# Performance work log

Hardware: AMD Instinct MI355X
Metric: run time of the kernel (lower is better)

The kernel has to match this reference:

```python
import jax, jax.numpy as jnp
import numpy as np

N = 256
FEAT = 1024           # box_head.fc7.out_features
HID_REL = 256         # RelationProposalNetwork hidden_dim
GCN_HID = 256         # gcn_hidden
HEADS = 4
NUM_PARTS = 20
OUT = NUM_PARTS + 1
TOPK = 3
IN_GCN = FEAT + 4


def setup_inputs() -> dict:
    key = jax.random.key(0)
    ks = jax.random.split(key, 16)
    features = jax.random.normal(ks[0], (N, FEAT), jnp.float32)
    # valid pixel-space boxes (x1, y1, x2, y2) inside an 800x800 image
    xy = jax.random.uniform(ks[1], (N, 2), jnp.float32, 0.0, 700.0)
    wh = jax.random.uniform(ks[2], (N, 2), jnp.float32, 8.0, 100.0)
    boxes = jnp.concatenate([xy, xy + wh], axis=1)
    s = 0.02
    W_fc1 = jax.random.normal(ks[3], (2 * FEAT + 4, HID_REL), jnp.float32) * s
    b_fc1 = jnp.zeros((HID_REL,), jnp.float32)
    W_fc2 = jax.random.normal(ks[4], (HID_REL, 1), jnp.float32) * s
    b_fc2 = jnp.zeros((1,), jnp.float32)
    W1 = jax.random.normal(ks[5], (IN_GCN, HEADS * GCN_HID), jnp.float32) * s
    a_src1 = jax.random.normal(ks[6], (HEADS, GCN_HID), jnp.float32) * s
    a_dst1 = jax.random.normal(ks[7], (HEADS, GCN_HID), jnp.float32) * s
    b1 = jnp.zeros((HEADS * GCN_HID,), jnp.float32)
    W2 = jax.random.normal(ks[8], (HEADS * GCN_HID, OUT), jnp.float32) * s
    a_src2 = jax.random.normal(ks[9], (1, OUT), jnp.float32) * s
    a_dst2 = jax.random.normal(ks[10], (1, OUT), jnp.float32) * s
    b2 = jnp.zeros((OUT,), jnp.float32)
    return {
        "features": features, "boxes": boxes,
        "W_fc1": W_fc1, "b_fc1": b_fc1, "W_fc2": W_fc2, "b_fc2": b_fc2,
        "W1": W1, "a_src1": a_src1, "a_dst1": a_dst1, "b1": b1,
        "W2": W2, "a_src2": a_src2, "a_dst2": a_dst2, "b2": b2,
        "img_h": 800, "img_w": 800,
    }


def _gat_layer(x, W, a_src, a_dst, bias, s, t, n, heads, ch):
    # PyG GATConv: message flows edge_index[0] (s) -> edge_index[1] (t),
    # softmax over incoming edges of each target node t.
    h = (x @ W).reshape(n, heads, ch)                       # [n, H, C]
    e = jax.nn.leaky_relu(
        jnp.einsum("ehc,hc->eh", h[s], a_src)
        + jnp.einsum("ehc,hc->eh", h[t], a_dst), 0.2)        # [E, H]
    m = jnp.full((n, heads), -1e30, e.dtype).at[t].max(e)    # segment max
    p = jnp.exp(e - m[t])
    denom = jax.ops.segment_sum(p, t, num_segments=n)
    alpha = p / denom[t]                                     # [E, H]
    out = jax.ops.segment_sum(alpha[:, :, None] * h[s], t, num_segments=n)
    return out.reshape(n, heads * ch) + bias


def _forward(features, boxes, W_fc1, b_fc1, W_fc2, b_fc2,
             W1, a_src1, a_dst1, b1, W2, a_src2, a_dst2, b2, img_h, img_w):
    n = features.shape[0]
    # --- RelationProposalNetwork: dense O(N^2) pairwise MLP ---
    f1 = jnp.broadcast_to(features[:, None, :], (n, n, FEAT))
    f2 = jnp.broadcast_to(features[None, :, :], (n, n, FEAT))
    geom = jnp.abs(boxes[:, None, :] - boxes[None, :, :])    # [n, n, 4]
    pair = jnp.concatenate([f1, f2, geom], axis=-1)          # [n, n, 2052]
    hid = jax.nn.relu(pair @ W_fc1 + b_fc1)                  # [n, n, 256]
    rel = (hid @ W_fc2 + b_fc2)[..., 0]                      # [n, n]
    # --- top-k graph construction (drop first = self, as in source) ---
    idx = jax.lax.top_k(rel, TOPK + 1)[1][:, 1:]             # [n, topk]
    s_e = jnp.repeat(jnp.arange(n), TOPK)                    # edge_index[0]
    t_e = idx.reshape(-1)                                    # edge_index[1]
    loops = jnp.arange(n)                                    # GATConv add_self_loops
    s_e = jnp.concatenate([s_e, loops])
    t_e = jnp.concatenate([t_e, loops])
    # --- normalized box geometry node features ---
    scale = jnp.array([img_w, img_h, img_w, img_h], jnp.float32)
    nb = boxes / scale
    geomn = jnp.stack([nb[:, 0], nb[:, 1], nb[:, 2] - nb[:, 0], nb[:, 3] - nb[:, 1]], axis=1)
    gcn_in = jnp.concatenate([features, geomn], axis=1)      # [n, 1028]
    # --- AttentionalGCN: GAT(heads=4) -> ReLU -> GAT(heads=1) ---
    h1 = jax.nn.relu(_gat_layer(gcn_in, W1, a_src1, a_dst1, b1, s_e, t_e, n, HEADS, GCN_HID))
    logits = _gat_layer(h1, W2, a_src2, a_dst2, b2, s_e, t_e, n, 1, OUT)
    return logits


def reference(features, boxes, W_fc1, b_fc1, W_fc2, b_fc2,
              W1, a_src1, a_dst1, b1, W2, a_src2, a_dst2, b2, img_h, img_w):
    logits = _forward(features, boxes, W_fc1, b_fc1, W_fc2, b_fc2,
                      W1, a_src1, a_dst1, b1, W2, a_src2, a_dst2, b2, img_h, img_w)
    labels = jnp.argmax(logits, axis=1)
    return logits, labels
```

## Files before the change

kernel.cpp:

```cpp
#include <hip/hip_runtime.h>
#include <math.h>

#define NN 256
#define FEAT 1024
#define HIDR 256
#define HEADS 4
#define GCNH 256
#define M1 1024
#define OUTC 21
#define MAXDEG (NN + 1)
#define KC 16
#define KCH (FEAT / KC)
#define RB 16
#define FCOLS 1536

__device__ __forceinline__ void st_wt4(float* p, float4 v) {
    union { float4 f; unsigned long long u[2]; } cv; cv.f = v;
    __hip_atomic_store((unsigned long long*)p, cv.u[0],
                       __ATOMIC_RELAXED, __HIP_MEMORY_SCOPE_AGENT);
    __hip_atomic_store((unsigned long long*)p + 1, cv.u[1],
                       __ATOMIC_RELAXED, __HIP_MEMORY_SCOPE_AGENT);
}
__device__ __forceinline__ void st_wtf(float* p, float v) {
    __hip_atomic_store((unsigned*)p, __float_as_uint(v),
                       __ATOMIC_RELAXED, __HIP_MEMORY_SCOPE_AGENT);
}
__device__ __forceinline__ void st_wti(int* p, int v) {
    __hip_atomic_store(p, v, __ATOMIC_RELAXED, __HIP_MEMORY_SCOPE_AGENT);
}

__global__ __launch_bounds__(256) void k_big(
        const float* __restrict__ feat, const float* __restrict__ Wfc1,
        const float* __restrict__ W1, float* __restrict__ P,
        unsigned* bar) {
    if (blockIdx.x == 0 && blockIdx.y == 0 && blockIdx.z == 0 &&
        threadIdx.x == 0)
        __hip_atomic_store(bar, 0u, __ATOMIC_RELAXED, __HIP_MEMORY_SCOPE_AGENT);
    __shared__ float fS[RB][KCH];
    int rg = blockIdx.x, cgy = blockIdx.y, kc = blockIdx.z;
    int tid = threadIdx.x;
    int r0 = rg * RB, k0 = kc * KCH;
    for (int x = tid; x < RB * KCH; x += 256) {
        int r = x >> 6, kk = x & (KCH - 1);
        fS[r][kk] = feat[(size_t)(r0 + r) * FEAT + k0 + kk];
    }
    __syncthreads();
    int gc = cgy * 512 + tid * 2;
    const float* pW;
    int ld;
    if (gc < 256)      { pW = Wfc1 + (size_t)k0 * HIDR + gc;                  ld = HIDR; }
    else if (gc < 512) { pW = Wfc1 + (size_t)(FEAT + k0) * HIDR + (gc - 256); ld = HIDR; }
    else               { pW = W1   + (size_t)k0 * M1 + (gc - 512);            ld = M1;   }
    float2 acc[RB];
#pragma unroll
    for (int r = 0; r < RB; r++) { acc[r].x = 0.f; acc[r].y = 0.f; }
    float2 w0 = *(const float2*)(pW);
    float2 w1 = *(const float2*)(pW + ld);
    float2 w2 = *(const float2*)(pW + 2 * ld);
    float2 w3 = *(const float2*)(pW + 3 * ld);
    for (int kk = 0; kk < KCH; kk += 4) {
        pW += 4 * ld;
        float2 n0 = *(const float2*)(pW);
        float2 n1 = *(const float2*)(pW + ld);
        float2 n2 = *(const float2*)(pW + 2 * ld);
        float2 n3 = *(const float2*)(pW + 3 * ld);
#pragma unroll
        for (int r = 0; r < RB; r++) {
            float4 f = *(const float4*)&fS[r][kk];
            acc[r].x = fmaf(f.x, w0.x, acc[r].x); acc[r].y = fmaf(f.x, w0.y, acc[r].y);
            acc[r].x = fmaf(f.y, w1.x, acc[r].x); acc[r].y = fmaf(f.y, w1.y, acc[r].y);
            acc[r].x = fmaf(f.z, w2.x, acc[r].x); acc[r].y = fmaf(f.z, w2.y, acc[r].y);
            acc[r].x = fmaf(f.w, w3.x, acc[r].x); acc[r].y = fmaf(f.w, w3.y, acc[r].y);
        }
        w0 = n0; w1 = n1; w2 = n2; w3 = n3;
    }
    float* Pp = P + ((size_t)kc * NN + r0) * FCOLS + gc;
#pragma unroll
    for (int r = 0; r < RB; r++)
        *(float2*)(Pp + (size_t)r * FCOLS) = acc[r];
}

__device__ __forceinline__ void gsync(unsigned* bar, unsigned expected) {
    __syncthreads();
    if (threadIdx.x == 0) {
        __hip_atomic_fetch_add(bar, 1u, __ATOMIC_RELAXED,
                               __HIP_MEMORY_SCOPE_AGENT);
        while (__hip_atomic_load(bar, __ATOMIC_RELAXED,
                                 __HIP_MEMORY_SCOPE_AGENT) < expected)
            __builtin_amdgcn_s_sleep(16);
        __builtin_amdgcn_fence(__ATOMIC_ACQUIRE, "agent");
    }
    __syncthreads();
}

__global__ __launch_bounds__(512, 4) void k_fused(
        const float* __restrict__ P, const float* __restrict__ bfc1,
        const float* __restrict__ boxes, const int* __restrict__ imh,
        const int* __restrict__ imw, const float* __restrict__ W1,
        const float* __restrict__ as1, const float* __restrict__ ad1,
        const float* __restrict__ Wfc1, const float* __restrict__ Wfc2,
        const float* __restrict__ b1, const float* __restrict__ W2,
        const float* __restrict__ as2, const float* __restrict__ ad2,
        const float* __restrict__ b2,
        float* __restrict__ BT4, float* __restrict__ hpre,
        float* __restrict__ es1, float* __restrict__ ed1,
        int* __restrict__ idxTop, float* __restrict__ h2,
        float* __restrict__ es2, float* __restrict__ ed2,
        unsigned* bar, float* __restrict__ out) {
    __shared__ float gS[4];
    __shared__ float As[HIDR], w2s[HIDR];
    __shared__ float wg0[HIDR], wg1[HIDR], wg2[HIDR], wg3[HIDR];
    __shared__ float sval[512];
    __shared__ unsigned long long swk[8];
    __shared__ int win;
    __shared__ int pfx[NN];
    __shared__ int lst[MAXDEG];
    __shared__ int dgS;
    __shared__ float sc[MAXDEG * 4];
    __shared__ float mh[4], dh[4];
    __shared__ float sh[M1];
    __shared__ float part[24 * OUTC];
    __shared__ float h2row[OUTC];
    __shared__ float scD[MAXDEG];
    __shared__ float md[2];
    __shared__ float lv[OUTC];

    int row = blockIdx.x, tid = threadIdx.x;

    int c4 = tid * 4;
    bool actA = (tid < 384);
    float4 s4;
    if (actA) {
        const float* p = P + (size_t)row * FCOLS + c4;
        const size_t str = (size_t)NN * FCOLS;
        float4 a0 = *(const float4*)(p);
        float4 a1 = *(const float4*)(p + str);
        float4 a2 = *(const float4*)(p + 2 * str);
        float4 a3 = *(const float4*)(p + 3 * str);
#pragma unroll
        for (int q = 4; q < KC; q += 4) {
            float4 t0 = *(const float4*)(p + (size_t)q * str);
            float4 t1 = *(const float4*)(p + (size_t)(q + 1) * str);
            float4 t2 = *(const float4*)(p + (size_t)(q + 2) * str);
            float4 t3 = *(const float4*)(p + (size_t)(q + 3) * str);
            a0.x += t0.x; a0.y += t0.y; a0.z += t0.z; a0.w += t0.w;
            a1.x += t1.x; a1.y += t1.y; a1.z += t1.z; a1.w += t1.w;
            a2.x += t2.x; a2.y += t2.y; a2.z += t2.z; a2.w += t2.w;
            a3.x += t3.x; a3.y += t3.y; a3.z += t3.z; a3.w += t3.w;
        }
        s4.x = (a0.x + a1.x) + (a2.x + a3.x);
        s4.y = (a0.y + a1.y) + (a2.y + a3.y);
        s4.z = (a0.z + a1.z) + (a2.z + a3.z);
        s4.w = (a0.w + a1.w) + (a2.w + a3.w);
    }
    if (tid == 0) {
        float w = (float)imw[0], h = (float)imh[0];
        float x1 = boxes[row * 4 + 0] / w, y1 = boxes[row * 4 + 1] / h;
        float x2 = boxes[row * 4 + 2] / w, y2 = boxes[row * 4 + 3] / h;
        gS[0] = x1; gS[1] = y1; gS[2] = x2 - x1; gS[3] = y2 - y1;
    }
    __syncthreads();
    if (actA) {
        if (c4 < 256) {
            float4 b = *(const float4*)(bfc1 + c4);
            s4.x += b.x; s4.y += b.y; s4.z += b.z; s4.w += b.w;
            *(float4*)(&As[c4]) = s4;
        } else if (c4 < 512) {
            int kk = c4 - 256;
            st_wt4(BT4 + (size_t)(kk >> 2) * (NN * 4) + row * 4, s4);
        } else {
            int ch = c4 - 512;
            float g0 = gS[0], g1 = gS[1], g2 = gS[2], g3 = gS[3];
            float4 wv;
            wv = *(const float4*)(W1 + (size_t)(FEAT + 0) * M1 + ch);
            s4.x = fmaf(g0, wv.x, s4.x); s4.y = fmaf(g0, wv.y, s4.y);
            s4.z = fmaf(g0, wv.z, s4.z); s4.w = fmaf(g0, wv.w, s4.w);
            wv = *(const float4*)(W1 + (size_t)(FEAT + 1) * M1 + ch);
            s4.x = fmaf(g1, wv.x, s4.x); s4.y = fmaf(g1, wv.y, s4.y);
            s4.z = fmaf(g1, wv.z, s4.z); s4.w = fmaf(g1, wv.w, s4.w);
            wv = *(const float4*)(W1 + (size_t)(FEAT + 2) * M1 + ch);
            s4.x = fmaf(g2, wv.x, s4.x); s4.y = fmaf(g2, wv.y, s4.y);
            s4.z = fmaf(g2, wv.z, s4.z); s4.w = fmaf(g2, wv.w, s4.w);
            wv = *(const float4*)(W1 + (size_t)(FEAT + 3) * M1 + ch);
            s4.x = fmaf(g3, wv.x, s4.x); s4.y = fmaf(g3, wv.y, s4.y);
            s4.z = fmaf(g3, wv.z, s4.z); s4.w = fmaf(g3, wv.w, s4.w);
            st_wt4(hpre + (size_t)row * M1 + ch, s4);
            float4 a = *(const float4*)(as1 + ch);
            float4 b = *(const float4*)(ad1 + ch);
            float ps = s4.x * a.x + s4.y * a.y + s4.z * a.z + s4.w * a.w;
            float pd = s4.x * b.x + s4.y * b.y + s4.z * b.z + s4.w * b.w;
#pragma unroll
            for (int o = 32; o > 0; o >>= 1) {
                ps += __shfl_down(ps, o);
                pd += __shfl_down(pd, o);
            }
            if ((tid & 63) == 0) {
                int head = (tid - 128) >> 6;
                st_wtf(es1 + row * 4 + head, ps);
                st_wtf(ed1 + row * 4 + head, pd);
            }
        }
    }

    gsync(bar, NN);

    if (tid < 256) {
        w2s[tid] = Wfc2[tid];
        wg0[tid] = Wfc1[(size_t)(2 * FEAT + 0) * HIDR + tid];
    } else {
        int q = tid - 256;
        wg1[q] = Wfc1[(size_t)(2 * FEAT + 1) * HIDR + q];
        wg2[q] = Wfc1[(size_t)(2 * FEAT + 2) * HIDR + q];
        wg3[q] = Wfc1[(size_t)(2 * FEAT + 3) * HIDR + q];
    }
    int j = tid & 255, half = tid >> 8;
    float bi0 = boxes[row * 4 + 0], bi1 = boxes[row * 4 + 1];
    float bi2 = boxes[row * 4 + 2], bi3 = boxes[row * 4 + 3];
    float g0 = fabsf(bi0 - boxes[j * 4 + 0]);
    float g1 = fabsf(bi1 - boxes[j * 4 + 1]);
    float g2 = fabsf(bi2 - boxes[j * 4 + 2]);
    float g3 = fabsf(bi3 - boxes[j * 4 + 3]);
    __syncthreads();
    {
        int k0 = half * 128;
        const float* pB = BT4 + (size_t)(k0 >> 2) * (NN * 4) + j * 4;
        float acc = 0.f;
#pragma unroll 4
        for (int kk = k0; kk < k0 + 128; kk += 4) {
            float4 a4 = *(const float4*)&As[kk];
            float4 w4 = *(const float4*)&w2s[kk];
            float4 q0 = *(const float4*)&wg0[kk];
            float4 q1 = *(const float4*)&wg1[kk];
            float4 q2 = *(const float4*)&wg2[kk];
            float4 q3 = *(const float4*)&wg3[kk];
            float4 b4 = *(const float4*)pB;
            pB += NN * 4;
            float v;
            v = a4.x + b4.x; v = fmaf(g0, q0.x, v); v = fmaf(g1, q1.x, v);
            v = fmaf(g2, q2.x, v); v = fmaf(g3, q3.x, v);
            acc = fmaf(fmaxf(v, 0.f), w4.x, acc);
            v = a4.y + b4.y; v = fmaf(g0, q0.y, v); v = fmaf(g1, q1.y, v);
            v = fmaf(g2, q2.y, v); v = fmaf(g3, q3.y, v);
            acc = fmaf(fmaxf(v, 0.f), w4.y, acc);
            v = a4.z + b4.z; v = fmaf(g0, q0.z, v); v = fmaf(g1, q1.z, v);
            v = fmaf(g2, q2.z, v); v = fmaf(g3, q3.z, v);
            acc = fmaf(fmaxf(v, 0.f), w4.z, acc);
            v = a4.w + b4.w; v = fmaf(g0, q0.w, v); v = fmaf(g1, q1.w, v);
            v = fmaf(g2, q2.w, v); v = fmaf(g3, q3.w, v);
            acc = fmaf(fmaxf(v, 0.f), w4.w, acc);
        }
        sval[tid] = acc;
    }
    __syncthreads();
    if (tid < 256) sval[tid] = sval[tid] + sval[tid + 256];
    __syncthreads();
    for (int r = 0; r < 4; r++) {
        unsigned long long key = 0ULL;
        if (tid < 256) {
            unsigned u = __float_as_uint(sval[tid]);
            u = (u & 0x80000000u) ? ~u : (u | 0x80000000u);
            key = ((unsigned long long)u << 32) | (unsigned)(NN - 1 - tid);
        }
#pragma unroll
        for (int o = 32; o > 0; o >>= 1) {
            unsigned long long nk = __shfl_down(key, o);
            if (nk > key) key = nk;
        }
        if ((tid & 63) == 0) swk[tid >> 6] = key;
        __syncthreads();
        if (tid == 0) {
            unsigned long long m = swk[0];
#pragma unroll
            for (int q = 1; q < 8; q++) if (swk[q] > m) m = swk[q];
            int wj = NN - 1 - (int)(m & 0xFFFFFFFFu);
            win = wj;
            if (r > 0) st_wti(idxTop + row * 3 + (r - 1), wj);
        }
        __syncthreads();
        if (tid == win) sval[tid] = -1e38f;
        __syncthreads();
    }

    gsync(bar, 2 * NN);

    int f = 0;
    if (tid < 256) {
        f = (idxTop[tid * 3 + 0] == row) | (idxTop[tid * 3 + 1] == row)
          | (idxTop[tid * 3 + 2] == row);
        pfx[tid] = f;
    }
    __syncthreads();
    for (int o = 1; o < NN; o <<= 1) {
        int add = 0;
        if (tid < 256 && tid >= o) add = pfx[tid - o];
        __syncthreads();
        if (tid < 256) pfx[tid] += add;
        __syncthreads();
    }
    if (tid < 256 && f) lst[pfx[tid] - 1] = tid;
    if (tid == NN - 1) {
        int d = pfx[NN - 1];
        lst[d] = row;
        dgS = d + 1;
    }
    __syncthreads();
    int dg = dgS;
    for (int p = tid; p < dg * 4; p += 512) {
        int e = p >> 2, hq = p & 3;
        int s = lst[e];
        float v = es1[s * 4 + hq] + ed1[row * 4 + hq];
        sc[p] = v >= 0.f ? v : 0.2f * v;
    }
    __syncthreads();
    {
        int hq = tid & 3;
        float lm = -1e30f;
        for (int e = tid >> 2; e < dg; e += 128)
            lm = fmaxf(lm, sc[e * 4 + hq]);
        sval[tid] = lm;
        __syncthreads();
        for (int o = 256; o >= 4; o >>= 1) {
            if (tid < o) sval[tid] = fmaxf(sval[tid], sval[tid + o]);
            __syncthreads();
        }
        if (tid < 4) mh[tid] = sval[tid];
        __syncthreads();
        float m = mh[hq];
        float lsum = 0.f;
        for (int e = tid >> 2; e < dg; e += 128) {
            float pv = expf(sc[e * 4 + hq] - m);
            sc[e * 4 + hq] = pv;
            lsum += pv;
        }
        sval[tid] = lsum;
        __syncthreads();
        for (int o = 256; o >= 4; o >>= 1) {
            if (tid < o) sval[tid] += sval[tid + o];
            __syncthreads();
        }
        if (tid < 4) dh[tid] = sval[tid];
        __syncthreads();
        for (int p = tid; p < dg * 4; p += 512)
            sc[p] = sc[p] / dh[p & 3];
    }
    __syncthreads();
    {
        int col = tid & 255, hh = (tid >> 8) * 2;
        float acc0 = 0.f, acc1 = 0.f;
        int e = 0;
        for (; e + 8 <= dg; e += 8) {
            float v0[8], v1[8];
#pragma unroll
            for (int u = 0; u < 8; u++) {
                const float* hs = hpre + (size_t)lst[e + u] * M1;
                v0[u] = hs[hh * GCNH + col];
                v1[u] = hs[(hh + 1) * GCNH + col];
            }
#pragma unroll
            for (int u = 0; u < 8; u++) {
                acc0 = fmaf(sc[(e + u) * 4 + hh],     v0[u], acc0);
                acc1 = fmaf(sc[(e + u) * 4 + hh + 1], v1[u], acc1);
            }
        }
        for (; e < dg; e++) {
            const float* hs = hpre + (size_t)lst[e] * M1;
            acc0 = fmaf(sc[e * 4 + hh],     hs[hh * GCNH + col],       acc0);
            acc1 = fmaf(sc[e * 4 + hh + 1], hs[(hh + 1) * GCNH + col], acc1);
        }
        int c0 = hh * GCNH + col, c1 = (hh + 1) * GCNH + col;
        sh[c0] = fmaxf(acc0 + b1[c0], 0.f);
        sh[c1] = fmaxf(acc1 + b1[c1], 0.f);
    }
    __syncthreads();
    if (tid < 504) {
        int o = tid % OUTC, pq = tid / OUTC;
        float a2 = 0.f;
        for (int d = pq; d < M1; d += 24)
            a2 = fmaf(sh[d], W2[d * OUTC + o], a2);
        part[pq * OUTC + o] = a2;
    }
    __syncthreads();
    if (tid < OUTC) {
        float ssum = 0.f;
        for (int pq = 0; pq < 24; pq++) ssum += part[pq * OUTC + tid];
        st_wtf(h2 + row * OUTC + tid, ssum);
        h2row[tid] = ssum;
    }
    __syncthreads();
    if (tid == 0) {
        float ssum = 0.f, dd = 0.f;
        for (int k = 0; k < OUTC; k++) {
            ssum = fmaf(h2row[k], as2[k], ssum);
            dd = fmaf(h2row[k], ad2[k], dd);
        }
        st_wtf(es2 + row, ssum);
        st_wtf(ed2 + row, dd);
    }

    gsync(bar, 3 * NN);

    int dgT = dgS;
    float edt = ed2[row];
    for (int p = tid; p < dgT; p += 512) {
        int s = lst[p];
        float v = es2[s] + edt;
        scD[p] = v >= 0.f ? v : 0.2f * v;
    }
    __syncthreads();
    {
        float lm = -1e30f;
        for (int p = tid; p < dgT; p += 512) lm = fmaxf(lm, scD[p]);
        sval[tid] = lm;
        __syncthreads();
        for (int o = 256; o >= 1; o >>= 1) {
            if (tid < o) sval[tid] = fmaxf(sval[tid], sval[tid + o]);
            __syncthreads();
        }
        if (tid == 0) md[0] = sval[0];
        __syncthreads();
        float m = md[0];
        float lsum = 0.f;
        for (int p = tid; p < dgT; p += 512) {
            float pv = expf(scD[p] - m);
            scD[p] = pv;
            lsum += pv;
        }
        sval[tid] = lsum;
        __syncthreads();
        for (int o = 256; o >= 1; o >>= 1) {
            if (tid < o) sval[tid] += sval[tid + o];
            __syncthreads();
        }
        if (tid == 0) md[1] = sval[0];
        __syncthreads();
    }
    if (tid < 504) {
        int o = tid % OUTC, eg = tid / OUTC;
        float acc = 0.f;
        for (int e = eg; e < dgT; e += 24) {
            int s = lst[e];
            acc = fmaf(scD[e], h2[(size_t)s * OUTC + o], acc);
        }
        part[eg * OUTC + o] = acc;
    }
    __syncthreads();
    if (tid < OUTC) {
        float ssum = 0.f;
        for (int eg = 0; eg < 24; eg++) ssum += part[eg * OUTC + tid];
        float v = ssum / md[1] + b2[tid];
        out[row * OUTC + tid] = v;
        lv[tid] = v;
    }
    __syncthreads();
    if (tid == 0) {
        int best = 0;
        float bv = lv[0];
        for (int o = 1; o < OUTC; o++)
            if (lv[o] > bv) { bv = lv[o]; best = o; }
        out[NN * OUTC + row] = (float)best;
    }
}

extern "C" void kernel_launch(void* const* d_in, const int* in_sizes, int n_in,
                              void* d_out, int out_size, void* d_ws,
                              size_t ws_size, hipStream_t stream) {
    const float* feat  = (const float*)d_in[0];
    const float* boxes = (const float*)d_in[1];
    const float* Wfc1  = (const float*)d_in[2];
    const float* bfc1  = (const float*)d_in[3];
    const float* Wfc2  = (const float*)d_in[4];
    const float* bfc2  = (const float*)d_in[5];   (void)bfc2;
    const float* W1    = (const float*)d_in[6];
    const float* as1   = (const float*)d_in[7];
    const float* ad1   = (const float*)d_in[8];
    const float* b1    = (const float*)d_in[9];
    const float* W2    = (const float*)d_in[10];
    const float* as2   = (const float*)d_in[11];
    const float* ad2   = (const float*)d_in[12];
    const float* b2    = (const float*)d_in[13];
    const int*   imh   = (const int*)d_in[14];
    const int*   imw   = (const int*)d_in[15];

    float* ws = (float*)d_ws;
    float* P     = ws;  ws += KC * NN * FCOLS;
    float* BT4   = ws;  ws += NN * HIDR;
    float* hpre  = ws;  ws += NN * M1;
    float* es1   = ws;  ws += NN * 4;
    float* ed1   = ws;  ws += NN * 4;
    float* h2    = ws;  ws += NN * OUTC;
    float* es2   = ws;  ws += NN;
    float* ed2   = ws;  ws += NN;
    int* idxTop  = (int*)ws;  ws += NN * 3;
    unsigned* bar = (unsigned*)ws;

    float* out = (float*)d_out;

    k_big<<<dim3(NN / RB, 3, KC), 256, 0, stream>>>(feat, Wfc1, W1, P, bar);
    k_fused<<<NN, 512, 0, stream>>>(P, bfc1, boxes, imh, imw, W1, as1, ad1,
                                    Wfc1, Wfc2, b1, W2, as2, ad2, b2,
                                    BT4, hpre, es1, ed1, idxTop, h2, es2, ed2,
                                    bar, out);
}
```

Baseline: 157.6 us.

## Fuse split-K GEMM into persistent kernel and use wave-level reductions

The separate split-K GEMM kernel becomes the first phase of the persistent cooperative kernel, with an extra grid barrier; each block now reads features straight from global memory instead of staging them in LDS, and handles three column groups. The barrier is reset with a memset instead of inside the first kernel. The barrier spin sleep is shortened, and the shared-memory tree reductions and prefix scan are replaced by wave shuffles and ballot/popcount. This removes one launch and many __syncthreads, but adds a grid barrier and changes the GEMM tiling and memory access pattern.

New measurement: 186.2 us. +18.1%, slower.

```diff
diff --git a/kernel.cpp b/kernel.cpp
--- a/kernel.cpp
+++ b/kernel.cpp
@@ -4,7 +4,6 @@
 #define NN 256
 #define FEAT 1024
 #define HIDR 256
-#define HEADS 4
 #define GCNH 256
 #define M1 1024
 #define OUTC 21
@@ -29,57 +28,6 @@
     __hip_atomic_store(p, v, __ATOMIC_RELAXED, __HIP_MEMORY_SCOPE_AGENT);
 }
 
-__global__ __launch_bounds__(256) void k_big(
-        const float* __restrict__ feat, const float* __restrict__ Wfc1,
-        const float* __restrict__ W1, float* __restrict__ P,
-        unsigned* bar) {
-    if (blockIdx.x == 0 && blockIdx.y == 0 && blockIdx.z == 0 &&
-        threadIdx.x == 0)
-        __hip_atomic_store(bar, 0u, __ATOMIC_RELAXED, __HIP_MEMORY_SCOPE_AGENT);
-    __shared__ float fS[RB][KCH];
-    int rg = blockIdx.x, cgy = blockIdx.y, kc = blockIdx.z;
-    int tid = threadIdx.x;
-    int r0 = rg * RB, k0 = kc * KCH;
-    for (int x = tid; x < RB * KCH; x += 256) {
-        int r = x >> 6, kk = x & (KCH - 1);
-        fS[r][kk] = feat[(size_t)(r0 + r) * FEAT + k0 + kk];
-    }
-    __syncthreads();
-    int gc = cgy * 512 + tid * 2;
-    const float* pW;
-    int ld;
-    if (gc < 256)      { pW = Wfc1 + (size_t)k0 * HIDR + gc;                  ld = HIDR; }
-    else if (gc < 512) { pW = Wfc1 + (size_t)(FEAT + k0) * HIDR + (gc - 256); ld = HIDR; }
-    else               { pW = W1   + (size_t)k0 * M1 + (gc - 512);            ld = M1;   }
-    float2 acc[RB];
-#pragma unroll
-    for (int r = 0; r < RB; r++) { acc[r].x = 0.f; acc[r].y = 0.f; }
-    float2 w0 = *(const float2*)(pW);
-    float2 w1 = *(const float2*)(pW + ld);
-    float2 w2 = *(const float2*)(pW + 2 * ld);
-    float2 w3 = *(const float2*)(pW + 3 * ld);
-    for (int kk = 0; kk < KCH; kk += 4) {
-        pW += 4 * ld;
-        float2 n0 = *(const float2*)(pW);
-        float2 n1 = *(const float2*)(pW + ld);
-        float2 n2 = *(const float2*)(pW + 2 * ld);
-        float2 n3 = *(const float2*)(pW + 3 * ld);
-#pragma unroll
-        for (int r = 0; r < RB; r++) {
-            float4 f = *(const float4*)&fS[r][kk];
-            acc[r].x = fmaf(f.x, w0.x, acc[r].x); acc[r].y = fmaf(f.x, w0.y, acc[r].y);
-            acc[r].x = fmaf(f.y, w1.x, acc[r].x); acc[r].y = fmaf(f.y, w1.y, acc[r].y);
-            acc[r].x = fmaf(f.z, w2.x, acc[r].x); acc[r].y = fmaf(f.z, w2.y, acc[r].y);
-            acc[r].x = fmaf(f.w, w3.x, acc[r].x); acc[r].y = fmaf(f.w, w3.y, acc[r].y);
-        }
-        w0 = n0; w1 = n1; w2 = n2; w3 = n3;
-    }
-    float* Pp = P + ((size_t)kc * NN + r0) * FCOLS + gc;
-#pragma unroll
-    for (int r = 0; r < RB; r++)
-        *(float2*)(Pp + (size_t)r * FCOLS) = acc[r];
-}
-
 __device__ __forceinline__ void gsync(unsigned* bar, unsigned expected) {
     __syncthreads();
     if (threadIdx.x == 0) {
@@ -87,45 +35,91 @@
                                __HIP_MEMORY_SCOPE_AGENT);
         while (__hip_atomic_load(bar, __ATOMIC_RELAXED,
                                  __HIP_MEMORY_SCOPE_AGENT) < expected)
-            __builtin_amdgcn_s_sleep(16);
+            __builtin_amdgcn_s_sleep(2);
         __builtin_amdgcn_fence(__ATOMIC_ACQUIRE, "agent");
     }
     __syncthreads();
 }
 
-__global__ __launch_bounds__(512, 4) void k_fused(
-        const float* __restrict__ P, const float* __restrict__ bfc1,
-        const float* __restrict__ boxes, const int* __restrict__ imh,
-        const int* __restrict__ imw, const float* __restrict__ W1,
+__global__ __launch_bounds__(512, 4) void k_all(
+        const float* __restrict__ feat, const float* __restrict__ boxes,
+        const float* __restrict__ Wfc1, const float* __restrict__ bfc1,
+        const float* __restrict__ Wfc2, const float* __restrict__ W1,
         const float* __restrict__ as1, const float* __restrict__ ad1,
-        const float* __restrict__ Wfc1, const float* __restrict__ Wfc2,
         const float* __restrict__ b1, const float* __restrict__ W2,
         const float* __restrict__ as2, const float* __restrict__ ad2,
-        const float* __restrict__ b2,
-        float* __restrict__ BT4, float* __restrict__ hpre,
-        float* __restrict__ es1, float* __restrict__ ed1,
-        int* __restrict__ idxTop, float* __restrict__ h2,
-        float* __restrict__ es2, float* __restrict__ ed2,
-        unsigned* bar, float* __restrict__ out) {
+        const float* __restrict__ b2, const int* __restrict__ imh,
+        const int* __restrict__ imw,
+        float* __restrict__ P, float* __restrict__ BT4,
+        float* __restrict__ hpre, float* __restrict__ es1,
+        float* __restrict__ ed1, int* __restrict__ idxTop,
+        float* __restrict__ h2, float* __restrict__ es2,
+        float* __restrict__ ed2, unsigned* bar, float* __restrict__ out) {
     __shared__ float gS[4];
     __shared__ float As[HIDR], w2s[HIDR];
     __shared__ float wg0[HIDR], wg1[HIDR], wg2[HIDR], wg3[HIDR];
     __shared__ float sval[512];
     __shared__ unsigned long long swk[8];
     __shared__ int win;
-    __shared__ int pfx[NN];
+    __shared__ int pfxw[4];
     __shared__ int lst[MAXDEG];
     __shared__ int dgS;
     __shared__ float sc[MAXDEG * 4];
-    __shared__ float mh[4], dh[4];
     __shared__ float sh[M1];
     __shared__ float part[24 * OUTC];
     __shared__ float h2row[OUTC];
     __shared__ float scD[MAXDEG];
-    __shared__ float md[2];
     __shared__ float lv[OUTC];
 
-    int row = blockIdx.x, tid = threadIdx.x;
+    int b = blockIdx.x, tid = threadIdx.x;
+
+    {
+        int rg = b & 15, kc = b >> 4;
+        int r0 = rg * RB, k0 = kc * KCH;
+        const float* p0 = (tid < 256)
+            ? Wfc1 + (size_t)k0 * HIDR + tid
+            : Wfc1 + (size_t)(FEAT + k0) * HIDR + (tid - 256);
+        const float* p1 = W1 + (size_t)k0 * M1 + tid;
+        const float* p2 = p1 + 512;
+        float acc0[RB], acc1[RB], acc2[RB];
+#pragma unroll
+        for (int r = 0; r < RB; r++) { acc0[r] = 0.f; acc1[r] = 0.f; acc2[r] = 0.f; }
+        const float* fbp = feat + (size_t)r0 * FEAT + k0;
+        for (int kb = 0; kb < KCH; kb += 8) {
+            float w0[8], w1[8], w2[8];
+#pragma unroll
+            for (int k = 0; k < 8; k++) {
+                w0[k] = p0[(size_t)k * HIDR];
+                w1[k] = p1[(size_t)k * M1];
+                w2[k] = p2[(size_t)k * M1];
+            }
+            p0 += 8 * HIDR; p1 += 8 * M1; p2 += 8 * M1;
+#pragma unroll
+            for (int r = 0; r < RB; r++) {
+                const float* fr = fbp + (size_t)r * FEAT + kb;
+                float4 fa = *(const float4*)(fr);
+                float4 fc = *(const float4*)(fr + 4);
+                float fv[8] = {fa.x, fa.y, fa.z, fa.w, fc.x, fc.y, fc.z, fc.w};
+#pragma unroll
+                for (int k = 0; k < 8; k++) {
+                    acc0[r] = fmaf(fv[k], w0[k], acc0[r]);
+                    acc1[r] = fmaf(fv[k], w1[k], acc1[r]);
+                    acc2[r] = fmaf(fv[k], w2[k], acc2[r]);
+                }
+            }
+        }
+        float* Pp = P + ((size_t)kc * NN + r0) * FCOLS;
+#pragma unroll
+        for (int r = 0; r < RB; r++) {
+            st_wtf(Pp + (size_t)r * FCOLS + tid,        acc0[r]);
+            st_wtf(Pp + (size_t)r * FCOLS + 512 + tid,  acc1[r]);
+            st_wtf(Pp + (size_t)r * FCOLS + 1024 + tid, acc2[r]);
+        }
+    }
+
+    gsync(bar, NN);
+
+    int row = b;
 
     int c4 = tid * 4;
     bool actA = (tid < 384);
@@ -162,8 +156,8 @@
     __syncthreads();
     if (actA) {
         if (c4 < 256) {
-            float4 b = *(const float4*)(bfc1 + c4);
-            s4.x += b.x; s4.y += b.y; s4.z += b.z; s4.w += b.w;
+            float4 bv = *(const float4*)(bfc1 + c4);
+            s4.x += bv.x; s4.y += bv.y; s4.z += bv.z; s4.w += bv.w;
             *(float4*)(&As[c4]) = s4;
         } else if (c4 < 512) {
             int kk = c4 - 256;
@@ -186,9 +180,9 @@
             s4.z = fmaf(g3, wv.z, s4.z); s4.w = fmaf(g3, wv.w, s4.w);
             st_wt4(hpre + (size_t)row * M1 + ch, s4);
             float4 a = *(const float4*)(as1 + ch);
-            float4 b = *(const float4*)(ad1 + ch);
+            float4 bv = *(const float4*)(ad1 + ch);
             float ps = s4.x * a.x + s4.y * a.y + s4.z * a.z + s4.w * a.w;
-            float pd = s4.x * b.x + s4.y * b.y + s4.z * b.z + s4.w * b.w;
+            float pd = s4.x * bv.x + s4.y * bv.y + s4.z * bv.z + s4.w * bv.w;
 #pragma unroll
             for (int o = 32; o > 0; o >>= 1) {
                 ps += __shfl_down(ps, o);
@@ -202,7 +196,7 @@
         }
     }
 
-    gsync(bar, NN);
+    gsync(bar, 2 * NN);
 
     if (tid < 256) {
         w2s[tid] = Wfc2[tid];
@@ -281,67 +275,64 @@
         __syncthreads();
     }
 
-    gsync(bar, 2 * NN);
+    gsync(bar, 3 * NN);
 
     int f = 0;
-    if (tid < 256) {
+    if (tid < 256)
         f = (idxTop[tid * 3 + 0] == row) | (idxTop[tid * 3 + 1] == row)
           | (idxTop[tid * 3 + 2] == row);
-        pfx[tid] = f;
-    }
-    __syncthreads();
-    for (int o = 1; o < NN; o <<= 1) {
-        int add = 0;
-        if (tid < 256 && tid >= o) add = pfx[tid - o];
-        __syncthreads();
-        if (tid < 256) pfx[tid] += add;
-        __syncthreads();
-    }
-    if (tid < 256 && f) lst[pfx[tid] - 1] = tid;
-    if (tid == NN - 1) {
-        int d = pfx[NN - 1];
-        lst[d] = row;
-        dgS = d + 1;
+    unsigned long long bm = __ballot(f);
+    int lane = tid & 63, wv6 = tid >> 6;
+    int rank = __popcll(bm & ((1ULL << lane) - 1ULL));
+    if (tid < 256 && lane == 0) pfxw[wv6] = __popcll(bm);
+    __syncthreads();
+    {
+        int base = 0;
+#pragma unroll
+        for (int w = 0; w < 4; w++) base += (w < wv6) ? pfxw[w] : 0;
+        if (tid < 256 && f) lst[base + rank] = tid;
+    }
+    if (tid == 0) {
+        int tot = pfxw[0] + pfxw[1] + pfxw[2] + pfxw[3];
+        lst[tot] = row;
+        dgS = tot + 1;
     }
     __syncthreads();
     int dg = dgS;
     for (int p = tid; p < dg * 4; p += 512) {
-        int e = p >> 2, hq = p & 3;
+        int e = p >> 2, hq2 = p & 3;
         int s = lst[e];
-        float v = es1[s * 4 + hq] + ed1[row * 4 + hq];
+        float v = es1[s * 4 + hq2] + ed1[row * 4 + hq2];
         sc[p] = v >= 0.f ? v : 0.2f * v;
     }
     __syncthreads();
-    {
-        int hq = tid & 3;
+    int hq = tid & 3;
+    {
         float lm = -1e30f;
         for (int e = tid >> 2; e < dg; e += 128)
             lm = fmaxf(lm, sc[e * 4 + hq]);
-        sval[tid] = lm;
-        __syncthreads();
-        for (int o = 256; o >= 4; o >>= 1) {
-            if (tid < o) sval[tid] = fmaxf(sval[tid], sval[tid + o]);
-            __syncthreads();
-        }
-        if (tid < 4) mh[tid] = sval[tid];
-        __syncthreads();
-        float m = mh[hq];
-        float lsum = 0.f;
+#pragma unroll
+        for (int o = 4; o <= 32; o <<= 1) lm = fmaxf(lm, __shfl_xor(lm, o));
+        if (lane < 4) sval[wv6 * 4 + hq] = lm;
+        __syncthreads();
+        float m = sval[hq];
+#pragma unroll
+        for (int w = 1; w < 8; w++) m = fmaxf(m, sval[w * 4 + hq]);
+        float ls = 0.f;
         for (int e = tid >> 2; e < dg; e += 128) {
             float pv = expf(sc[e * 4 + hq] - m);
             sc[e * 4 + hq] = pv;
-            lsum += pv;
-        }
-        sval[tid] = lsum;
-        __syncthreads();
-        for (int o = 256; o >= 4; o >>= 1) {
-            if (tid < o) sval[tid] += sval[tid + o];
-            __syncthreads();
-        }
-        if (tid < 4) dh[tid] = sval[tid];
-        __syncthreads();
-        for (int p = tid; p < dg * 4; p += 512)
-            sc[p] = sc[p] / dh[p & 3];
+            ls += pv;
+        }
+#pragma unroll
+        for (int o = 4; o <= 32; o <<= 1) ls += __shfl_xor(ls, o);
+        if (lane < 4) sval[32 + wv6 * 4 + hq] = ls;
+        __syncthreads();
+        float den = sval[32 + hq];
+#pragma unroll
+        for (int w = 1; w < 8; w++) den += sval[32 + w * 4 + hq];
+        for (int e = tid >> 2; e < dg; e += 128)
+            sc[e * 4 + hq] = sc[e * 4 + hq] / den;
     }
     __syncthreads();
     {
@@ -397,7 +388,7 @@
         st_wtf(ed2 + row, dd);
     }
 
-    gsync(bar, 3 * NN);
+    gsync(bar, 4 * NN);
 
     int dgT = dgS;
     float edt = ed2[row];
@@ -410,46 +401,44 @@
     {
         float lm = -1e30f;
         for (int p = tid; p < dgT; p += 512) lm = fmaxf(lm, scD[p]);
-        sval[tid] = lm;
-        __syncthreads();
-        for (int o = 256; o >= 1; o >>= 1) {
-            if (tid < o) sval[tid] = fmaxf(sval[tid], sval[tid + o]);
-            __syncthreads();
-        }
-        if (tid == 0) md[0] = sval[0];
-        __syncthreads();
-        float m = md[0];
-        float lsum = 0.f;
+#pragma unroll
+        for (int o = 1; o <= 32; o <<= 1) lm = fmaxf(lm, __shfl_xor(lm, o));
+        if (lane == 0) sval[wv6] = lm;
+        __syncthreads();
+        float m = sval[0];
+#pragma unroll
+        for (int w = 1; w < 8; w++) m = fmaxf(m, sval[w]);
+        float ls = 0.f;
         for (int p = tid; p < dgT; p += 512) {
             float pv = expf(scD[p] - m);
             scD[p] = pv;
-            lsum += pv;
-        }
-        sval[tid] = lsum;
-        __syncthreads();
-        for (int o = 256; o >= 1; o >>= 1) {
-            if (tid < o) sval[tid] += sval[tid + o];
-            __syncthreads();
-        }
-        if (tid == 0) md[1] = sval[0];
-        __syncthreads();
-    }
-    if (tid < 504) {
-        int o = tid % OUTC, eg = tid / OUTC;
-        float acc = 0.f;
-        for (int e = eg; e < dgT; e += 24) {
-            int s = lst[e];
-            acc = fmaf(scD[e], h2[(size_t)s * OUTC + o], acc);
-        }
-        part[eg * OUTC + o] = acc;
-    }
-    __syncthreads();
-    if (tid < OUTC) {
-        float ssum = 0.f;
-        for (int eg = 0; eg < 24; eg++) ssum += part[eg * OUTC + tid];
-        float v = ssum / md[1] + b2[tid];
-        out[row * OUTC + tid] = v;
-        lv[tid] = v;
+            ls += pv;
+        }
+#pragma unroll
+        for (int o = 1; o <= 32; o <<= 1) ls += __shfl_xor(ls, o);
+        if (lane == 0) sval[8 + wv6] = ls;
+        __syncthreads();
+        float den = sval[8];
+#pragma unroll
+        for (int w = 1; w < 8; w++) den += sval[8 + w];
+        __syncthreads();
+        if (tid < 504) {
+            int o = tid % OUTC, eg = tid / OUTC;
+            float acc = 0.f;
+            for (int e = eg; e < dgT; e += 24) {
+                int s = lst[e];
+                acc = fmaf(scD[e], h2[(size_t)s * OUTC + o], acc);
+            }
+            part[eg * OUTC + o] = acc;
+        }
+        __syncthreads();
+        if (tid < OUTC) {
+            float ssum = 0.f;
+            for (int eg = 0; eg < 24; eg++) ssum += part[eg * OUTC + tid];
+            float v = ssum / den + b2[tid];
+            out[row * OUTC + tid] = v;
+            lv[tid] = v;
+        }
     }
     __syncthreads();
     if (tid == 0) {
@@ -490,14 +479,14 @@
     float* h2    = ws;  ws += NN * OUTC;
     float* es2   = ws;  ws += NN;
     float* ed2   = ws;  ws += NN;
-    int* idxTop  = (int*)ws;  ws += NN * 3;
-    unsigned* bar = (unsigned*)ws;
+    int* idxTop  = (int*)ws;
+    unsigned* bar = (unsigned*)(idxTop + NN * 3);
 
     float* out = (float*)d_out;
 
-    k_big<<<dim3(NN / RB, 3, KC), 256, 0, stream>>>(feat, Wfc1, W1, P, bar);
-    k_fused<<<NN, 512, 0, stream>>>(P, bfc1, boxes, imh, imw, W1, as1, ad1,
-                                    Wfc1, Wfc2, b1, W2, as2, ad2, b2,
-                                    BT4, hpre, es1, ed1, idxTop, h2, es2, ed2,
-                                    bar, out);
-}
+    hipMemsetAsync(bar, 0, sizeof(unsigned), stream);
+    k_all<<<NN, 512, 0, stream>>>(feat, boxes, Wfc1, bfc1, Wfc2, W1,
+                                  as1, ad1, b1, W2, as2, ad2, b2, imh, imw,
+                                  P, BT4, hpre, es1, ed1, idxTop,
+                                  h2, es2, ed2, bar, out);
+}
```
